# Performance work log

Measured on AMD Instinct MI355X. Metric: run time of the kernel, lower is better.

## Reference

```python
import jax, jax.numpy as jnp
import numpy as np

N_NODES = 50000
N_EDGES = 800000
D_IN = 128
H = 4
D_HEAD = 32
NEG_SLOPE = 0.2


def _weighted_agg(h, w, src, dst, n):
    # agg[dst] += h[src] * w  (DGL update_all with weighted_message/reduce)
    return jax.ops.segment_sum(h[src] * w[:, None], dst, num_segments=n)


def _gat_conv(h, W, al, ar, b, src, dst):
    # DGL GATConv (eval mode: dropout off), activation=None, bias=True
    n = h.shape[0]
    feat = (h @ W).reshape(n, H, D_HEAD)          # [N,H,D]
    el = jnp.sum(feat * al, axis=-1)               # [N,H]
    er = jnp.sum(feat * ar, axis=-1)               # [N,H]
    e = jax.nn.leaky_relu(el[src] + er[dst], NEG_SLOPE)  # [E,H]
    # edge softmax over incoming edges of each dst node, per head
    m = jax.ops.segment_max(e, dst, num_segments=n)      # [N,H]
    ee = jnp.exp(e - m[dst])
    s = jax.ops.segment_sum(ee, dst, num_segments=n)     # [N,H]
    alpha = ee / s[dst]                                   # [E,H]
    msg = feat[src] * alpha[:, :, None]                   # [E,H,D]
    rst = jax.ops.segment_sum(msg, dst, num_segments=n)   # [N,H,D]
    rst = rst + b.reshape(1, H, D_HEAD)
    return rst.reshape(n, H * D_HEAD)                     # flatten(1)


def setup_inputs() -> dict:
    key = jax.random.key(0)
    ks = jax.random.split(key, 12)
    inp = {
        "in_feat": jax.random.normal(ks[0], (N_NODES, D_IN), dtype=jnp.float32),
        "edge_weights": jax.random.uniform(ks[1], (N_EDGES,), dtype=jnp.float32),
        "W0": jax.random.normal(ks[2], (D_IN, H * D_HEAD), dtype=jnp.float32) * (1.0 / np.sqrt(D_IN)),
        "al0": jax.random.normal(ks[3], (H, D_HEAD), dtype=jnp.float32) * 0.1,
        "ar0": jax.random.normal(ks[4], (H, D_HEAD), dtype=jnp.float32) * 0.1,
        "b0": jnp.zeros((H * D_HEAD,), dtype=jnp.float32),
        "W1": jax.random.normal(ks[5], (H * D_HEAD, H * D_HEAD), dtype=jnp.float32) * (1.0 / np.sqrt(H * D_HEAD)),
        "al1": jax.random.normal(ks[6], (H, D_HEAD), dtype=jnp.float32) * 0.1,
        "ar1": jax.random.normal(ks[7], (H, D_HEAD), dtype=jnp.float32) * 0.1,
        "b1": jnp.zeros((H * D_HEAD,), dtype=jnp.float32),
        "src": jax.random.randint(ks[8], (N_EDGES,), 0, N_NODES, dtype=jnp.int32),
        "dst": jax.random.randint(ks[9], (N_EDGES,), 0, N_NODES, dtype=jnp.int32),
    }
    return inp


def reference(in_feat, edge_weights, W0, al0, ar0, b0, W1, al1, ar1, b1, src, dst):
    n = in_feat.shape[0]
    h = in_feat
    # hidden layer (layers[:-1]) with edge-weighted aggregation + residual + relu
    h_old = h
    h = h + _weighted_agg(h, edge_weights, src, dst, n)
    h = _gat_conv(h, W0, al0, ar0, b0, src, dst)
    h = h + h_old  # residual=True
    h = jax.nn.relu(h)
    # final layer
    h = h + _weighted_agg(h, edge_weights, src, dst, n)
    h = _gat_conv(h, W1, al1, ar1, b1, src, dst)
    return h
```

## Files before the change

### kernel.cpp

```cpp
#include <hip/hip_runtime.h>

#define NN 50000
#define NE 800000
#define D 128
#define NH 4
#define NB 391

typedef __attribute__((ext_vector_type(8))) short bf16x8;
typedef __attribute__((ext_vector_type(4))) float f32x4;

__device__ __forceinline__ float lrelu(float x){ return x > 0.f ? x : 0.2f*x; }
__device__ __forceinline__ float sel4(int h, float4 v){
  float r = v.x;
  r = (h==1)? v.y : r;
  r = (h==2)? v.z : r;
  r = (h==3)? v.w : r;
  return r;
}
__device__ __forceinline__ ushort f2bf(float f){
  union{ float f; uint i;} v; v.f=f;
  uint r = v.i + 0x7FFFu + ((v.i>>16)&1u);
  return (ushort)(r>>16);
}
__device__ __forceinline__ uint pack2bf(float x, float y){
  return (uint)f2bf(x) | ((uint)f2bf(y)<<16);
}
__device__ __forceinline__ float bflo(uint u){ return __uint_as_float(u<<16); }
__device__ __forceinline__ float bfhi(uint u){ return __uint_as_float(u & 0xffff0000u); }
__device__ __forceinline__ uint encf(float f){
  uint b = __float_as_uint(f);
  return (b & 0x80000000u) ? ~b : (b | 0x80000000u);
}
__device__ __forceinline__ float decf(uint e){
  return (e & 0x80000000u) ? __uint_as_float(e ^ 0x80000000u) : __uint_as_float(~e);
}


__global__ void k_bhist(const int* __restrict__ dst, int* __restrict__ bcnt){
  __shared__ int c[NB];
  int t = threadIdx.x;
  for (int i=t;i<NB;i+=256) c[i]=0;
  __syncthreads();
  int base = blockIdx.x*4096;
  #pragma unroll
  for (int k=0;k<16;k++){
    int i = base + k*256 + t;
    if (i<NE) atomicAdd(&c[dst[i]>>7], 1);
  }
  __syncthreads();
  for (int i=t;i<NB;i+=256){ int v=c[i]; if (v) atomicAdd(&bcnt[i], v); }
}

__global__ void k_bscan(const int* __restrict__ bcnt, int* __restrict__ boff, int* __restrict__ bcur){
  __shared__ int sd[512];
  int t = threadIdx.x;
  int own = (t<NB)? bcnt[t] : 0;
  sd[t] = own;
  __syncthreads();
  for (int off=1; off<512; off<<=1){
    int v = (t>=off)? sd[t-off] : 0;
    __syncthreads();
    sd[t] += v;
    __syncthreads();
  }
  if (t<NB){
    int excl = sd[t]-own;
    boff[t]=excl; bcur[t]=excl;
  }
  if (t==0) boff[NB]=NE;
}

__global__ void k_binscat(const int* __restrict__ src, const int* __restrict__ dst,
                          const float* __restrict__ w, int* __restrict__ bcur,
                          uint2* __restrict__ stg){
  __shared__ int cnt[NB];
  __shared__ int st[NB];
  int t = threadIdx.x;
  for (int i=t;i<NB;i+=256) cnt[i]=0;
  __syncthreads();
  int base = blockIdx.x*4096;
  #pragma unroll
  for (int k=0;k<16;k++){
    int i = base + k*256 + t;
    if (i<NE) atomicAdd(&cnt[dst[i]>>7], 1);
  }
  __syncthreads();
  for (int i=t;i<NB;i+=256){
    int c = cnt[i];
    st[i] = c ? atomicAdd(&bcur[i], c) : 0;
    cnt[i] = 0;
  }
  __syncthreads();
  #pragma unroll
  for (int k=0;k<16;k++){
    int i = base + k*256 + t;
    if (i<NE){
      int d = dst[i];
      int b = d>>7;
      int pos = st[b] + atomicAdd(&cnt[b], 1);
      stg[pos] = make_uint2((uint)src[i] | ((uint)d<<16), __float_as_uint(w[i]));
    }
  }
}

__global__ void k_bfinal(const uint2* __restrict__ stg, const int* __restrict__ boff,
                         int* __restrict__ offs, uint2* __restrict__ edge_s){
  int b = blockIdx.x, t = threadIdx.x;
  int beg = boff[b], end = boff[b+1];
  int node0 = b<<7;
  int nnode = NN - node0; if (nnode>128) nnode=128;
  __shared__ int cnt[128];
  __shared__ int cur[128];
  if (t<128) cnt[t]=0;
  __syncthreads();
  for (int j=beg+t; j<end; j+=256)
    atomicAdd(&cnt[(stg[j].x>>16)&127], 1);
  __syncthreads();
  int own = (t<128)? cnt[t] : 0;
  for (int off=1; off<128; off<<=1){
    int v = (t<128 && t>=off)? cnt[t-off] : 0;
    __syncthreads();
    if (t<128) cnt[t] += v;
    __syncthreads();
  }
  if (t<128){
    int excl = cnt[t]-own;
    cur[t] = beg + excl;
    if (t<nnode) offs[node0+t] = beg + excl;
  }
  if (b==NB-1 && t==0) offs[NN]=NE;
  __syncthreads();
  for (int j=beg+t; j<end; j+=256){
    uint2 v = stg[j];
    int pos = atomicAdd(&cur[(v.x>>16)&127], 1);
    edge_s[pos] = v;
  }
}


__global__ void k_cvt(const float* __restrict__ in, uint* __restrict__ out16, int n2){
  int i = blockIdx.x*256 + threadIdx.x;
  if (i < n2){
    float2 f = *(const float2*)&in[(size_t)i*2];
    out16[i] = pack2bf(f.x, f.y);
  }
}

__global__ void k_cvtW(const float* __restrict__ W, uint* __restrict__ Wt){
  int i = blockIdx.x*256 + threadIdx.x;
  if (i < 128*64){
    int n = i>>6, k2 = i&63;
    float a = W[(size_t)(2*k2)*128 + n];
    float b = W[(size_t)(2*k2+1)*128 + n];
    Wt[i] = pack2bf(a,b);
  }
}

__global__ void k_wagg(const float* __restrict__ hinF, const uint* __restrict__ hin16,
                       const int* __restrict__ offs, const uint2* __restrict__ edge_s,
                       uint* __restrict__ xout16){
  int node = (blockIdx.x*256 + threadIdx.x)>>6;
  int lane = threadIdx.x & 63;
  if (node>=NN) return;
  int beg=offs[node], end=offs[node+1];
  int half = lane>>5, li = lane&31;
  float a0=0.f,a1=0.f,a2=0.f,a3=0.f;
  if (half==0){
    if (hinF){
      float4 s4 = *(const float4*)&hinF[(size_t)node*D + li*4];
      a0=s4.x; a1=s4.y; a2=s4.z; a3=s4.w;
    } else {
      uint2 su = *(const uint2*)&hin16[(size_t)node*64 + li*2];
      a0=bflo(su.x); a1=bfhi(su.x); a2=bflo(su.y); a3=bfhi(su.y);
    }
  }
  for (int cb=beg; cb<end; cb+=64){
    int n = end-cb; if (n>64) n=64;
    int idx = cb + (lane<n ? lane : n-1);
    uint2 ed = edge_s[idx];
    int sp = (int)(ed.x & 0xffffu);
    float wp = __uint_as_float(ed.y);
    int iters = (n+1)>>1;
    for (int i0=0; i0<iters; i0+=8){
      uint2 u[8]; float wk[8];
      #pragma unroll
      for (int k=0;k<8;k++){
        int q = 2*(i0+k) + half;
        int sj = __shfl(sp, q & 63);
        float wq = __shfl(wp, q & 63);
        wk[k] = (q<n)? wq : 0.f;
        u[k] = *(const uint2*)&hin16[(size_t)sj*64 + li*2];
      }
      #pragma unroll
      for (int k=0;k<8;k++){
        a0 = fmaf(bflo(u[k].x), wk[k], a0);
        a1 = fmaf(bfhi(u[k].x), wk[k], a1);
        a2 = fmaf(bflo(u[k].y), wk[k], a2);
        a3 = fmaf(bfhi(u[k].y), wk[k], a3);
      }
    }
  }
  a0 += __shfl_xor(a0,32); a1 += __shfl_xor(a1,32);
  a2 += __shfl_xor(a2,32); a3 += __shfl_xor(a3,32);
  if (half==0){
    uint2 o; o.x = pack2bf(a0,a1); o.y = pack2bf(a2,a3);
    *(uint2*)&xout16[(size_t)node*64 + li*2] = o;
  }
}

__global__ __launch_bounds__(256) void k_gemm(const uint* __restrict__ X16, const uint* __restrict__ Wt16,
    const float* __restrict__ al, const float* __restrict__ ar,
    uint* __restrict__ feat16, float4* __restrict__ el4o, float4* __restrict__ er4o,
    uint* __restrict__ gmax_u){
  __shared__ uint sX[128*64];
  __shared__ uint sW[128*64];
  __shared__ float sgm[4][4];
  int t = threadIdx.x;
  int row0 = blockIdx.x*128;
  #pragma unroll
  for (int i=0;i<8;i++){
    int idx = t + 256*i;
    int r = idx>>4, cb = idx&15;
    int gr = row0 + r;
    uint4 v = make_uint4(0u,0u,0u,0u);
    if (gr < NN) v = *(const uint4*)&X16[(size_t)gr*64 + cb*4];
    *(uint4*)&sX[r*64 + ((cb*4) ^ ((r&7)<<2))] = v;
  }
  #pragma unroll
  for (int i=0;i<8;i++){
    int idx = t + 256*i;
    int r = idx>>4, cb = idx&15;
    uint4 v = *(const uint4*)&Wt16[(size_t)r*64 + cb*4];
    *(uint4*)&sW[r*64 + ((cb*4) ^ ((r&7)<<2))] = v;
  }
  __syncthreads();
  int w = t>>6, l = t&63;
  int lr = l&15, lk = l>>4;
  f32x4 acc[2][8];
  #pragma unroll
  for (int rf=0;rf<2;rf++)
    #pragma unroll
    for (int cf=0;cf<8;cf++) acc[rf][cf] = (f32x4){0.f,0.f,0.f,0.f};
  #pragma unroll
  for (int ks=0; ks<4; ks++){
    int cb = ks*4 + lk;
    bf16x8 a[2], b[8];
    #pragma unroll
    for (int rf=0;rf<2;rf++){
      int r = w*32 + rf*16 + lr;
      a[rf] = *(const bf16x8*)&sX[r*64 + ((cb*4) ^ ((r&7)<<2))];
    }
    #pragma unroll
    for (int cf=0;cf<8;cf++){
      int r = cf*16 + lr;
      b[cf] = *(const bf16x8*)&sW[r*64 + ((cb*4) ^ ((r&7)<<2))];
    }
    #pragma unroll
    for (int rf=0;rf<2;rf++)
      #pragma unroll
      for (int cf=0;cf<8;cf++)
        acc[rf][cf] = __builtin_amdgcn_mfma_f32_16x16x32_bf16(a[rf], b[cf], acc[rf][cf], 0,0,0);
  }
  float al_v[8], ar_v[8];
  #pragma unroll
  for (int cf=0;cf<8;cf++){ al_v[cf]=al[cf*16+lr]; ar_v[cf]=ar[cf*16+lr]; }
  float gm0=-3e38f,gm1=-3e38f,gm2=-3e38f,gm3=-3e38f;
  #pragma unroll
  for (int rf=0;rf<2;rf++){
    #pragma unroll
    for (int reg=0;reg<4;reg++){
      int grow = row0 + w*32 + rf*16 + lk*4 + reg;
      float eh[4]={0.f,0.f,0.f,0.f}, fh[4]={0.f,0.f,0.f,0.f};
      #pragma unroll
      for (int cf=0;cf<8;cf++){
        float v = acc[rf][cf][reg];
        eh[cf>>1] = fmaf(v, al_v[cf], eh[cf>>1]);
        fh[cf>>1] = fmaf(v, ar_v[cf], fh[cf>>1]);
      }
      #pragma unroll
      for (int off=1; off<16; off<<=1){
        #pragma unroll
        for (int h=0;h<4;h++){
          eh[h] += __shfl_xor(eh[h], off);
          fh[h] += __shfl_xor(fh[h], off);
        }
      }
      if (lr==0 && grow<NN){
        el4o[grow] = make_float4(eh[0],eh[1],eh[2],eh[3]);
        er4o[grow] = make_float4(fh[0],fh[1],fh[2],fh[3]);
      }
      if (grow<NN){
        gm0=fmaxf(gm0,eh[0]); gm1=fmaxf(gm1,eh[1]);
        gm2=fmaxf(gm2,eh[2]); gm3=fmaxf(gm3,eh[3]);
      }
      #pragma unroll
      for (int cf=0;cf<8;cf++){
        float v = acc[rf][cf][reg];
        float pv = __shfl_xor(v, 1);
        if (!(lr&1) && grow<NN)
          feat16[(size_t)grow*64 + ((cf*16+lr)>>1)] = pack2bf(v, pv);
      }
    }
  }
  #pragma unroll
  for (int off=1; off<64; off<<=1){
    gm0=fmaxf(gm0,__shfl_xor(gm0,off));
    gm1=fmaxf(gm1,__shfl_xor(gm1,off));
    gm2=fmaxf(gm2,__shfl_xor(gm2,off));
    gm3=fmaxf(gm3,__shfl_xor(gm3,off));
  }
  if (l==0){ sgm[w][0]=gm0; sgm[w][1]=gm1; sgm[w][2]=gm2; sgm[w][3]=gm3; }
  __syncthreads();
  if (t==0){
    float m0=fmaxf(fmaxf(sgm[0][0],sgm[1][0]),fmaxf(sgm[2][0],sgm[3][0]));
    float m1=fmaxf(fmaxf(sgm[0][1],sgm[1][1]),fmaxf(sgm[2][1],sgm[3][1]));
    float m2=fmaxf(fmaxf(sgm[0][2],sgm[1][2]),fmaxf(sgm[2][2],sgm[3][2]));
    float m3=fmaxf(fmaxf(sgm[0][3],sgm[1][3]),fmaxf(sgm[2][3],sgm[3][3]));
    atomicMax(&gmax_u[0], encf(m0));
    atomicMax(&gmax_u[1], encf(m1));
    atomicMax(&gmax_u[2], encf(m2));
    atomicMax(&gmax_u[3], encf(m3));
  }
}

template<int FINAL>
__global__ void k_gat(const uint* __restrict__ feat16, const float4* __restrict__ el4,
                      const float4* __restrict__ er4, const uint* __restrict__ gmax_u,
                      const float* __restrict__ bias, const int* __restrict__ offs,
                      const uint2* __restrict__ edge_s, const float* __restrict__ resid,
                      float* __restrict__ outF, uint* __restrict__ out16){
  int node = (blockIdx.x*256 + threadIdx.x)>>6;
  int lane = threadIdx.x & 63;
  if (node>=NN) return;
  int beg=offs[node], end=offs[node+1];
  int half = lane>>5, li = lane&31;
  int hF = li>>3;
  int hp = lane & 3;
  int eidx = lane>>2;
  float4 erv = er4[node];
  uint4 g = *(const uint4*)gmax_u;
  float4 m4 = make_float4(lrelu(decf(g.x)+erv.x), lrelu(decf(g.y)+erv.y),
                          lrelu(decf(g.z)+erv.z), lrelu(decf(g.w)+erv.w));
  float mh  = sel4(hp, m4);
  float erh = sel4(hp, erv);
  float s_acc = 0.f;
  float a0=0.f,a1=0.f,a2=0.f,a3=0.f;
  for (int cb=beg; cb<end; cb+=16){
    int n = end-cb; if (n>16) n=16;
    int jj = cb + (eidx<n ? eidx : n-1);
    uint2 ed = edge_s[jj];
    int sp = (int)(ed.x & 0xffffu);
    float4 ev = el4[sp];
    float e = __expf(lrelu(sel4(hp,ev)+erh) - mh);
    e = (eidx<n) ? e : 0.f;
    s_acc += e;
    uint2 u[8]; float eh[8];
    #pragma unroll
    for (int k=0;k<8;k++){
      int bidx = (2*k + half)<<2;
      int sj = __shfl(sp, bidx);
      eh[k] = __shfl(e, bidx + hF);
      u[k] = *(const uint2*)&feat16[(size_t)sj*64 + li*2];
    }
    #pragma unroll
    for (int k=0;k<8;k++){
      a0 = fmaf(bflo(u[k].x), eh[k], a0);
      a1 = fmaf(bfhi(u[k].x), eh[k], a1);
      a2 = fmaf(bflo(u[k].y), eh[k], a2);
      a3 = fmaf(bfhi(u[k].y), eh[k], a3);
    }
  }
  s_acc += __shfl_xor(s_acc,4);
  s_acc += __shfl_xor(s_acc,8);
  s_acc += __shfl_xor(s_acc,16);
  s_acc += __shfl_xor(s_acc,32);
  float sh = __shfl(s_acc, hF);
  a0 += __shfl_xor(a0,32); a1 += __shfl_xor(a1,32);
  a2 += __shfl_xor(a2,32); a3 += __shfl_xor(a3,32);
  if (half==0){
    float inv = (end>beg)? 1.f/sh : 0.f;
    float4 bv = *(const float4*)&bias[li*4];
    float r0 = a0*inv + bv.x;
    float r1 = a1*inv + bv.y;
    float r2 = a2*inv + bv.z;
    float r3 = a3*inv + bv.w;
    if (FINAL==0){
      float4 rs = *(const float4*)&resid[(size_t)node*D + li*4];
      r0 = fmaxf(r0+rs.x, 0.f);
      r1 = fmaxf(r1+rs.y, 0.f);
      r2 = fmaxf(r2+rs.z, 0.f);
      r3 = fmaxf(r3+rs.w, 0.f);
      uint2 o16; o16.x = pack2bf(r0,r1); o16.y = pack2bf(r2,r3);
      *(uint2*)&out16[(size_t)node*64 + li*2] = o16;
    } else {
      *(float4*)&outF[(size_t)node*D + li*4] = make_float4(r0,r1,r2,r3);
    }
  }
}

extern "C" void kernel_launch(void* const* d_in, const int* in_sizes, int n_in,
                              void* d_out, int out_size, void* d_ws, size_t ws_size,
                              hipStream_t stream){
  const float* in_feat = (const float*)d_in[0];
  const float* ew  = (const float*)d_in[1];
  const float* W0  = (const float*)d_in[2];
  const float* al0 = (const float*)d_in[3];
  const float* ar0 = (const float*)d_in[4];
  const float* b0  = (const float*)d_in[5];
  const float* W1  = (const float*)d_in[6];
  const float* al1 = (const float*)d_in[7];
  const float* ar1 = (const float*)d_in[8];
  const float* b1  = (const float*)d_in[9];
  const int* src = (const int*)d_in[10];
  const int* dst = (const int*)d_in[11];
  float* out = (float*)d_out;

  char* p = (char*)d_ws;
  auto alloc = [&](size_t b)->void*{ void* r=(void*)p; p += ((b+255)&~(size_t)255); return r; };
  int*   offs   = (int*)alloc((size_t)(NN+1)*4);
  int*   bcnt   = (int*)alloc((size_t)NB*4);
  int*   boff   = (int*)alloc((size_t)(NB+1)*4);
  int*   bcur   = (int*)alloc((size_t)NB*4);
  uint2* stg    = (uint2*)alloc((size_t)NE*8);
  uint2* edge_s = (uint2*)alloc((size_t)NE*8);
  uint*  h16    = (uint*)alloc((size_t)NN*64*4);
  uint*  x16    = (uint*)alloc((size_t)NN*64*4);
  uint*  feat16 = (uint*)alloc((size_t)NN*64*4);
  uint*  Wt0    = (uint*)alloc((size_t)128*64*4);
  uint*  Wt1    = (uint*)alloc((size_t)128*64*4);
  float* el     = (float*)alloc((size_t)NN*NH*4);
  float* er     = (float*)alloc((size_t)NN*NH*4);
  uint*  gmax0  = (uint*)alloc(16);
  uint*  gmax1  = (uint*)alloc(16);

  hipMemsetAsync(bcnt, 0, (size_t)NB*4, stream);
  hipMemsetAsync(gmax0, 0, 16, stream);
  hipMemsetAsync(gmax1, 0, 16, stream);
  int nsb = (NE + 4095)/4096;
  k_bhist<<<nsb,256,0,stream>>>(dst, bcnt);
  k_bscan<<<1,512,0,stream>>>(bcnt, boff, bcur);
  k_binscat<<<nsb,256,0,stream>>>(src, dst, ew, bcur, stg);
  k_bfinal<<<NB,256,0,stream>>>(stg, boff, offs, edge_s);
  k_cvt<<<(NN*64+255)/256,256,0,stream>>>(in_feat, h16, NN*64);
  k_cvtW<<<(128*64+255)/256,256,0,stream>>>(W0, Wt0);
  k_cvtW<<<(128*64+255)/256,256,0,stream>>>(W1, Wt1);

  int nwb = (NN*64 + 255)/256;
  int ngb = (NN+127)/128;

  k_wagg<<<nwb,256,0,stream>>>(in_feat, h16, offs, edge_s, x16);
  k_gemm<<<ngb,256,0,stream>>>(x16, Wt0, al0, ar0, feat16, (float4*)el, (float4*)er, gmax0);
  k_gat<0><<<nwb,256,0,stream>>>(feat16, (const float4*)el, (const float4*)er, gmax0, b0,
                                 offs, edge_s, in_feat, nullptr, h16);
  k_wagg<<<nwb,256,0,stream>>>(nullptr, h16, offs, edge_s, x16);
  k_gemm<<<ngb,256,0,stream>>>(x16, Wt1, al1, ar1, feat16, (float4*)el, (float4*)er, gmax1);
  k_gat<1><<<nwb,256,0,stream>>>(feat16, (const float4*)el, (const float4*)er, gmax1, b1,
                                 offs, edge_s, nullptr, out, nullptr);
}
```

Baseline: 263.7 us.

## Fold attention projections into augmented weight matrix computed by MFMA

```diff
diff --git a/kernel.cpp b/kernel.cpp
--- a/kernel.cpp
+++ b/kernel.cpp
@@ -153,6 +153,28 @@
     float a = W[(size_t)(2*k2)*128 + n];
     float b = W[(size_t)(2*k2+1)*128 + n];
     Wt[i] = pack2bf(a,b);
+  }
+}
+
+__global__ void k_prep(const float* __restrict__ W0, const float* __restrict__ al0,
+                       const float* __restrict__ ar0, const float* __restrict__ W1,
+                       const float* __restrict__ al1, const float* __restrict__ ar1,
+                       uint* __restrict__ aug0, uint* __restrict__ aug1){
+  __shared__ float sv[128][4];
+  int b = blockIdx.x, t = threadIdx.x;
+  const float* W = (b<2)? W0 : W1;
+  const float* a = (b==0)? al0 : (b==1)? ar0 : (b==2)? al1 : ar1;
+  uint* o = (b<2)? aug0 : aug1;
+  int rbase = (b&1)? 132 : 128;
+  int d = t>>2, h = t&3;
+  float s = 0.f;
+  #pragma unroll
+  for (int i=0;i<32;i++) s += W[d*128 + h*32 + i] * a[h*32 + i];
+  sv[d][h] = s;
+  __syncthreads();
+  if (t<256){
+    int h2 = t>>6, k2 = t&63;
+    o[(rbase+h2)*64 + k2] = pack2bf(sv[2*k2][h2], sv[2*k2+1][h2]);
   }
 }
 
@@ -208,12 +230,11 @@
   }
 }
 
-__global__ __launch_bounds__(256) void k_gemm(const uint* __restrict__ X16, const uint* __restrict__ Wt16,
-    const float* __restrict__ al, const float* __restrict__ ar,
-    uint* __restrict__ feat16, float4* __restrict__ el4o, float4* __restrict__ er4o,
+__global__ __launch_bounds__(256) void k_gemm(const uint* __restrict__ X16, const uint* __restrict__ Wtaug,
+    uint* __restrict__ feat16, float* __restrict__ el, float* __restrict__ er,
     uint* __restrict__ gmax_u){
   __shared__ uint sX[128*64];
-  __shared__ uint sW[128*64];
+  __shared__ uint sW[144*64];
   __shared__ float sgm[4][4];
   int t = threadIdx.x;
   int row0 = blockIdx.x*128;
@@ -227,24 +248,27 @@
     *(uint4*)&sX[r*64 + ((cb*4) ^ ((r&7)<<2))] = v;
   }
   #pragma unroll
-  for (int i=0;i<8;i++){
+  for (int i=0;i<9;i++){
     int idx = t + 256*i;
     int r = idx>>4, cb = idx&15;
-    uint4 v = *(const uint4*)&Wt16[(size_t)r*64 + cb*4];
+    uint4 v = *(const uint4*)&Wtaug[(size_t)r*64 + cb*4];
     *(uint4*)&sW[r*64 + ((cb*4) ^ ((r&7)<<2))] = v;
   }
   __syncthreads();
   int w = t>>6, l = t&63;
   int lr = l&15, lk = l>>4;
   f32x4 acc[2][8];
-  #pragma unroll
-  for (int rf=0;rf<2;rf++)
+  f32x4 acc_e[2];
+  #pragma unroll
+  for (int rf=0;rf<2;rf++){
+    acc_e[rf] = (f32x4){0.f,0.f,0.f,0.f};
     #pragma unroll
     for (int cf=0;cf<8;cf++) acc[rf][cf] = (f32x4){0.f,0.f,0.f,0.f};
+  }
   #pragma unroll
   for (int ks=0; ks<4; ks++){
     int cb = ks*4 + lk;
-    bf16x8 a[2], b[8];
+    bf16x8 a[2], b[8], baug;
     #pragma unroll
     for (int rf=0;rf<2;rf++){
       int r = w*32 + rf*16 + lr;
@@ -255,71 +279,42 @@
       int r = cf*16 + lr;
       b[cf] = *(const bf16x8*)&sW[r*64 + ((cb*4) ^ ((r&7)<<2))];
     }
-    #pragma unroll
-    for (int rf=0;rf<2;rf++)
+    {
+      int r = 128 + lr;
+      baug = *(const bf16x8*)&sW[r*64 + ((cb*4) ^ ((r&7)<<2))];
+    }
+    #pragma unroll
+    for (int rf=0;rf<2;rf++){
       #pragma unroll
       for (int cf=0;cf<8;cf++)
         acc[rf][cf] = __builtin_amdgcn_mfma_f32_16x16x32_bf16(a[rf], b[cf], acc[rf][cf], 0,0,0);
-  }
-  float al_v[8], ar_v[8];
-  #pragma unroll
-  for (int cf=0;cf<8;cf++){ al_v[cf]=al[cf*16+lr]; ar_v[cf]=ar[cf*16+lr]; }
-  float gm0=-3e38f,gm1=-3e38f,gm2=-3e38f,gm3=-3e38f;
+      acc_e[rf] = __builtin_amdgcn_mfma_f32_16x16x32_bf16(a[rf], baug, acc_e[rf], 0,0,0);
+    }
+  }
+  ushort* f16s = (ushort*)feat16;
+  float gm = -3e38f;
   #pragma unroll
   for (int rf=0;rf<2;rf++){
     #pragma unroll
     for (int reg=0;reg<4;reg++){
       int grow = row0 + w*32 + rf*16 + lk*4 + reg;
-      float eh[4]={0.f,0.f,0.f,0.f}, fh[4]={0.f,0.f,0.f,0.f};
-      #pragma unroll
-      for (int cf=0;cf<8;cf++){
-        float v = acc[rf][cf][reg];
-        eh[cf>>1] = fmaf(v, al_v[cf], eh[cf>>1]);
-        fh[cf>>1] = fmaf(v, ar_v[cf], fh[cf>>1]);
+      if (grow < NN){
+        #pragma unroll
+        for (int cf=0;cf<8;cf++)
+          f16s[(size_t)grow*128 + cf*16 + lr] = f2bf(acc[rf][cf][reg]);
+        float v = acc_e[rf][reg];
+        if (lr<4){ el[grow*4 + lr] = v; gm = fmaxf(gm, v); }
+        else if (lr<8){ er[grow*4 + lr-4] = v; }
       }
-      #pragma unroll
-      for (int off=1; off<16; off<<=1){
-        #pragma unroll
-        for (int h=0;h<4;h++){
-          eh[h] += __shfl_xor(eh[h], off);
-          fh[h] += __shfl_xor(fh[h], off);
-        }
-      }
-      if (lr==0 && grow<NN){
-        el4o[grow] = make_float4(eh[0],eh[1],eh[2],eh[3]);
-        er4o[grow] = make_float4(fh[0],fh[1],fh[2],fh[3]);
-      }
-      if (grow<NN){
-        gm0=fmaxf(gm0,eh[0]); gm1=fmaxf(gm1,eh[1]);
-        gm2=fmaxf(gm2,eh[2]); gm3=fmaxf(gm3,eh[3]);
-      }
-      #pragma unroll
-      for (int cf=0;cf<8;cf++){
-        float v = acc[rf][cf][reg];
-        float pv = __shfl_xor(v, 1);
-        if (!(lr&1) && grow<NN)
-          feat16[(size_t)grow*64 + ((cf*16+lr)>>1)] = pack2bf(v, pv);
-      }
-    }
-  }
-  #pragma unroll
-  for (int off=1; off<64; off<<=1){
-    gm0=fmaxf(gm0,__shfl_xor(gm0,off));
-    gm1=fmaxf(gm1,__shfl_xor(gm1,off));
-    gm2=fmaxf(gm2,__shfl_xor(gm2,off));
-    gm3=fmaxf(gm3,__shfl_xor(gm3,off));
-  }
-  if (l==0){ sgm[w][0]=gm0; sgm[w][1]=gm1; sgm[w][2]=gm2; sgm[w][3]=gm3; }
-  __syncthreads();
-  if (t==0){
-    float m0=fmaxf(fmaxf(sgm[0][0],sgm[1][0]),fmaxf(sgm[2][0],sgm[3][0]));
-    float m1=fmaxf(fmaxf(sgm[0][1],sgm[1][1]),fmaxf(sgm[2][1],sgm[3][1]));
-    float m2=fmaxf(fmaxf(sgm[0][2],sgm[1][2]),fmaxf(sgm[2][2],sgm[3][2]));
-    float m3=fmaxf(fmaxf(sgm[0][3],sgm[1][3]),fmaxf(sgm[2][3],sgm[3][3]));
-    atomicMax(&gmax_u[0], encf(m0));
-    atomicMax(&gmax_u[1], encf(m1));
-    atomicMax(&gmax_u[2], encf(m2));
-    atomicMax(&gmax_u[3], encf(m3));
+    }
+  }
+  gm = fmaxf(gm, __shfl_xor(gm,16));
+  gm = fmaxf(gm, __shfl_xor(gm,32));
+  if (l<4) sgm[w][l] = gm;
+  __syncthreads();
+  if (t<4){
+    float m = fmaxf(fmaxf(sgm[0][t],sgm[1][t]), fmaxf(sgm[2][t],sgm[3][t]));
+    atomicMax(&gmax_u[t], encf(m));
   }
 }
 
@@ -426,8 +421,8 @@
   uint*  h16    = (uint*)alloc((size_t)NN*64*4);
   uint*  x16    = (uint*)alloc((size_t)NN*64*4);
   uint*  feat16 = (uint*)alloc((size_t)NN*64*4);
-  uint*  Wt0    = (uint*)alloc((size_t)128*64*4);
-  uint*  Wt1    = (uint*)alloc((size_t)128*64*4);
+  uint*  Wt0    = (uint*)alloc((size_t)144*64*4);
+  uint*  Wt1    = (uint*)alloc((size_t)144*64*4);
   float* el     = (float*)alloc((size_t)NN*NH*4);
   float* er     = (float*)alloc((size_t)NN*NH*4);
   uint*  gmax0  = (uint*)alloc(16);
@@ -436,6 +431,8 @@
   hipMemsetAsync(bcnt, 0, (size_t)NB*4, stream);
   hipMemsetAsync(gmax0, 0, 16, stream);
   hipMemsetAsync(gmax1, 0, 16, stream);
+  hipMemsetAsync(Wt0, 0, (size_t)144*64*4, stream);
+  hipMemsetAsync(Wt1, 0, (size_t)144*64*4, stream);
   int nsb = (NE + 4095)/4096;
   k_bhist<<<nsb,256,0,stream>>>(dst, bcnt);
   k_bscan<<<1,512,0,stream>>>(bcnt, boff, bcur);
@@ -444,16 +441,17 @@
   k_cvt<<<(NN*64+255)/256,256,0,stream>>>(in_feat, h16, NN*64);
   k_cvtW<<<(128*64+255)/256,256,0,stream>>>(W0, Wt0);
   k_cvtW<<<(128*64+255)/256,256,0,stream>>>(W1, Wt1);
+  k_prep<<<4,512,0,stream>>>(W0, al0, ar0, W1, al1, ar1, Wt0, Wt1);
 
   int nwb = (NN*64 + 255)/256;
   int ngb = (NN+127)/128;
 
   k_wagg<<<nwb,256,0,stream>>>(in_feat, h16, offs, edge_s, x16);
-  k_gemm<<<ngb,256,0,stream>>>(x16, Wt0, al0, ar0, feat16, (float4*)el, (float4*)er, gmax0);
+  k_gemm<<<ngb,256,0,stream>>>(x16, Wt0, feat16, el, er, gmax0);
   k_gat<0><<<nwb,256,0,stream>>>(feat16, (const float4*)el, (const float4*)er, gmax0, b0,
                                  offs, edge_s, in_feat, nullptr, h16);
   k_wagg<<<nwb,256,0,stream>>>(nullptr, h16, offs, edge_s, x16);
-  k_gemm<<<ngb,256,0,stream>>>(x16, Wt1, al1, ar1, feat16, (float4*)el, (float4*)er, gmax1);
+  k_gemm<<<ngb,256,0,stream>>>(x16, Wt1, feat16, el, er, gmax1);
   k_gat<1><<<nwb,256,0,stream>>>(feat16, (const float4*)el, (const float4*)er, gmax1, b1,
                                  offs, edge_s, nullptr, out, nullptr);
 }
```

New measurement: 234.8 us (median of 2 runs). 1.12x faster.
